# Kernel optimization log

Measured on AMD Instinct MI355X. Metric: run time of the kernel, lower is better.

Reference implementation:

```python
import jax, jax.numpy as jnp
import numpy as np

NUM_HEADS = 4
KEY_DIMS = 32  # c // num_heads


def rel_to_abs(x):
    # x: [B, N, W, 2W-1] relative logits -> [B, N, W, W] absolute logits
    b, n, w, _ = x.shape
    x = jnp.pad(x, ((0, 0), (0, 0), (0, 0), (0, 1)))           # [b,n,w,2w]
    x = x.reshape(b, n, w * 2 * w)
    x = jnp.pad(x, ((0, 0), (0, 0), (0, w - 1)))
    x = x.reshape(b, n, w + 1, 2 * w - 1)
    return x[:, :, :w, w - 1:]


def rel_logits_1d(q, rel_k):
    # q: [B, heads, X, Y, d], rel_k: [2Y-1, d] -> [B, heads, X, X, Y, Y]
    b, nh, xx, yy, d = q.shape
    rl = jnp.einsum('bhxyd,md->bhxym', q, rel_k)               # [b,h,x,y,2y-1]
    rl = rel_to_abs(rl.reshape(b, nh * xx, yy, 2 * yy - 1))    # [b,h*x,y,y]
    rl = rl.reshape(b, nh, xx, 1, yy, yy)
    return jnp.broadcast_to(rl, (b, nh, xx, xx, yy, yy))


def relative_position_bias(pos_q, pos_emb_h, pos_emb_w):
    # pos_q: [B, heads, H, W, d] -> bias [B, heads, H, W, H, W]
    rw = rel_logits_1d(pos_q, pos_emb_w)                        # [b,h,H,H,W,W]
    rw = rw.transpose(0, 1, 2, 4, 3, 5)                         # [b,h,H,W,H,W]
    rh = rel_logits_1d(pos_q.transpose(0, 1, 3, 2, 4), pos_emb_h)  # [b,h,W,W,H,H]
    rh = rh.transpose(0, 1, 4, 2, 5, 3)                         # [b,h,H,W,H,W]
    return rw + rh


def setup_inputs() -> dict:
    key = jax.random.key(0)
    k1, k2, k3, k4 = jax.random.split(key, 4)
    B, H, W, C = 2, 64, 64, 128
    qk_dims = NUM_HEADS * KEY_DIMS  # 128
    out_channels = C
    x = jax.random.normal(k1, (B, H, W, C), dtype=jnp.float32)
    w_qkv = jax.random.normal(k2, (C, 2 * qk_dims + out_channels), dtype=jnp.float32) * 0.05
    pos_emb_h = jax.random.normal(k3, (2 * H - 1, KEY_DIMS), dtype=jnp.float32) * 0.05
    pos_emb_w = jax.random.normal(k4, (2 * W - 1, KEY_DIMS), dtype=jnp.float32) * 0.05
    return {'x': x, 'w_qkv': w_qkv, 'pos_emb_h': pos_emb_h, 'pos_emb_w': pos_emb_w}


def reference(x, w_qkv, pos_emb_h, pos_emb_w):
    B, H, W, C = x.shape
    nh, kd = NUM_HEADS, KEY_DIMS
    qk_dims = nh * kd
    oc = C
    scale = 1.0 / float(kd) ** 0.5

    qkv = jnp.einsum('bhwc,cd->bhwd', x, w_qkv)                 # 1x1 conv, no bias
    q, k, v = jnp.split(qkv, [qk_dims, 2 * qk_dims], axis=-1)
    L = H * W
    q = q.reshape(B, L, nh, kd).transpose(0, 2, 1, 3)           # [B,nh,L,kd]
    k = k.reshape(B, L, nh, kd).transpose(0, 2, 1, 3)           # [B,nh,L,kd]
    v = v.reshape(B, L, nh, oc // nh).transpose(0, 2, 1, 3)     # [B,nh,L,dv]

    pos_q = q.reshape(B, nh, H, W, kd)
    pos = relative_position_bias(pos_q, pos_emb_h, pos_emb_w).reshape(B, nh, L, L)

    scores = jnp.einsum('bnqd,bnkd->bnqk', q, k) * scale + pos  # [B,nh,L,L]
    attn = jax.nn.softmax(scores, axis=-1)
    out = jnp.einsum('bnqk,bnkd->bnqd', attn, v)                # [B,nh,L,dv]
    out = out.transpose(0, 2, 1, 3).reshape(B, H, W, oc)
    return out
```

## Files before the change

### kernel.cpp

```cpp
#include <hip/hip_runtime.h>
#include <hip/hip_bf16.h>
#include <math.h>

#define B_  2
#define NH  4
#define HH  64
#define WW  64
#define KD  32
#define L_  4096
#define BN_ 8
#define LOG2E 1.4426950408889634f
#define KSCALE (0.17677669529663687f * 1.4426950408889634f)
#define FIXED_M 10.0f

typedef float    f32x4  __attribute__((ext_vector_type(4), may_alias));
typedef _Float16 half8  __attribute__((ext_vector_type(8), may_alias));
typedef _Float16 half4  __attribute__((ext_vector_type(4), may_alias));
typedef __fp16   fp16x2 __attribute__((ext_vector_type(2)));
typedef unsigned uint4v __attribute__((ext_vector_type(4), may_alias));

__device__ __forceinline__ float fexp2(float x) {
#if __has_builtin(__builtin_amdgcn_exp2f)
    return __builtin_amdgcn_exp2f(x);
#else
    return __expf(x * 0.69314718056f);
#endif
}

__device__ __forceinline__ unsigned pack2u(float a, float b) {
    fp16x2 t = __builtin_amdgcn_cvt_pkrtz(a, b);
    union { fp16x2 i; unsigned o; } u;
    u.i = t;
    return u.o;
}

__global__ __launch_bounds__(256) void qkv_gemm(const float* __restrict__ x,
                                                const float* __restrict__ w,
                                                _Float16* __restrict__ q_h,
                                                _Float16* __restrict__ k_h,
                                                _Float16* __restrict__ vt_h) {
    __shared__ __align__(16) char smem[34816];
    _Float16* xs  = (_Float16*)smem;
    _Float16* wsT = (_Float16*)(smem + 17408);

    const int mt = blockIdx.x % 128;
    const int nt = blockIdx.x / 128;
    const int m0 = mt * 64, n0 = nt * 64;
    const int tid = threadIdx.x;
    const int wv = tid >> 6, lane = tid & 63;
    const int l16 = lane & 15, quad = lane >> 4;

    #pragma unroll
    for (int i = 0; i < 8; i++) {
        const int idx = i * 256 + tid;
        const int row = idx >> 5, c4 = (idx & 31) * 4;
        const float4 v = *(const float4*)&x[(size_t)(m0 + row) * 128 + c4];
        half4 h;
        h[0] = (_Float16)v.x; h[1] = (_Float16)v.y;
        h[2] = (_Float16)v.z; h[3] = (_Float16)v.w;
        *(half4*)&xs[row * 136 + c4] = h;
    }
    #pragma unroll
    for (int i = 0; i < 8; i++) {
        const int idx = i * 256 + tid;
        const int k = idx >> 4, c4 = (idx & 15) * 4;
        const float4 v = *(const float4*)&w[(size_t)k * 384 + n0 + c4];
        wsT[(c4 + 0) * 136 + k] = (_Float16)v.x;
        wsT[(c4 + 1) * 136 + k] = (_Float16)v.y;
        wsT[(c4 + 2) * 136 + k] = (_Float16)v.z;
        wsT[(c4 + 3) * 136 + k] = (_Float16)v.w;
    }
    __syncthreads();

    f32x4 acc[4] = {{0.f,0.f,0.f,0.f},{0.f,0.f,0.f,0.f},
                    {0.f,0.f,0.f,0.f},{0.f,0.f,0.f,0.f}};
    half8 af[4];
    #pragma unroll
    for (int kc = 0; kc < 4; kc++)
        af[kc] = *(const half8*)&xs[(wv * 16 + l16) * 136 + kc * 32 + quad * 8];
    #pragma unroll
    for (int ns = 0; ns < 4; ns++)
        #pragma unroll
        for (int kc = 0; kc < 4; kc++) {
            const half8 bf = *(const half8*)&wsT[(ns * 16 + l16) * 136 + kc * 32 + quad * 8];
            acc[ns] = __builtin_amdgcn_mfma_f32_16x16x32_f16(af[kc], bf, acc[ns], 0, 0, 0);
        }

    const int which = n0 >> 7;
    const int nc = n0 & 127;
    const int b = m0 >> 12;
    if (which < 2) {
        _Float16* dst = (which == 0) ? q_h : k_h;
        const float mult = (which == 1) ? KSCALE : 1.0f;
        #pragma unroll
        for (int ns = 0; ns < 4; ns++) {
            const int col = nc + ns * 16 + l16;
            const int bn = b * NH + (col >> 5);
            const int d = col & 31;
            #pragma unroll
            for (int r = 0; r < 4; r++) {
                const int l = (m0 & 4095) + wv * 16 + quad * 4 + r;
                dst[((size_t)bn * L_ + l) * 32 + d] = (_Float16)(acc[ns][r] * mult);
            }
        }
    } else {
        __syncthreads();
        float* img = (float*)smem;
        #pragma unroll
        for (int ns = 0; ns < 4; ns++) {
            const int chan = ns * 16 + l16;
            const int h = chan >> 5, d = chan & 31;
            #pragma unroll
            for (int r = 0; r < 4; r++) {
                const int p = wv * 16 + quad * 4 + r;
                const int y = p >> 5, p32 = p & 31;
                const int q4 = (p32 >> 2) & 3;
                const int j = ((p32 >> 4) & 1) * 4 + (p32 & 3);
                const int fidx = h * 2048 + (y * 2 + (d >> 4)) * 512
                               + (q4 * 16 + (d & 15)) * 8 + j;
                img[fidx + (fidx >> 4)] = acc[ns][r];
            }
        }
        __syncthreads();
        const int ktg = (m0 & 4095) >> 6;
        #pragma unroll
        for (int h = 0; h < 2; h++) {
            const int head = (nc >> 5) + h;
            const int bn = b * NH + head;
            const int fbase = h * 2048 + tid * 8;
            const int sbase = fbase + (fbase >> 4);
            half8 o;
            #pragma unroll
            for (int e = 0; e < 8; e++) o[e] = (_Float16)img[sbase + e];
            *(half8*)(vt_h + (size_t)bn * 131072 + ktg * 2048 + tid * 8) = o;
        }
    }
}

__global__ __launch_bounds__(1024) void attn_mfma(
    const _Float16* __restrict__ q_h,
    const _Float16* __restrict__ k_h,
    const _Float16* __restrict__ vt_h,
    const float* __restrict__ emb_h,
    const float* __restrict__ emb_w,
    float* __restrict__ out)
{
    __shared__ __align__(16) char smem[66048];

    const int bi    = blockIdx.x;
    const int bn    = bi & 7;
    const int wpair = bi >> 3;
    const int tid   = threadIdx.x;
    const int wv    = tid >> 6;
    const int kh    = wv >> 3;
    const int ws    = wv & 7;
    const int qg    = ws >> 1;
    const int wo    = ws & 1;
    const int w1    = wpair * 2 + wo;
    const int lane  = tid & 63;
    const int l16   = lane & 15;
    const int quad  = lane >> 4;
    const int q0    = qg * 16;

    const _Float16* Kbase = k_h  + (size_t)bn * L_ * 32;
    const _Float16* Vtile = vt_h + (size_t)bn * 131072;

    const int Tt  = wv & 3;
    const int sC  = wv >> 2;
    const int khT = Tt & 1;
    const int isV = Tt >> 1;
    const _Float16* gstage = (isV ? Vtile : Kbase)
                           + (size_t)khT * 32 * 2048 + sC * 512 + lane * 8;
    const int ldsT = khT * 4096 + (isV
        ? (8192 + sC * 1024 + lane * 16)
        : ((sC * 16 + (lane >> 2)) * 64 + (((lane & 3) ^ ((lane >> 3) & 3)) << 4)));

    const uint4v stg0 = *(const uint4v*)gstage;

    float* Rw = (float*)(smem + 32768) + ws * 1040;

    const half8 aq = *(const half8*)(q_h +
        (((size_t)bn * L_ + (q0 + l16) * 64 + w1) * 32 + quad * 8));

    f32x4 qwT[4];
    #pragma unroll
    for (int sub = 0; sub < 4; sub++) {
        const float* ew = emb_w + (size_t)(sub * 16 + l16 - w1 + 63) * 32 + quad * 8;
        const float4 e0 = *(const float4*)ew;
        const float4 e1 = *(const float4*)(ew + 4);
        union { uint4v u; half8 h; } ua;
        ua.u[0] = pack2u(e0.x * LOG2E, e0.y * LOG2E);
        ua.u[1] = pack2u(e0.z * LOG2E, e0.w * LOG2E);
        ua.u[2] = pack2u(e1.x * LOG2E, e1.y * LOG2E);
        ua.u[3] = pack2u(e1.z * LOG2E, e1.w * LOG2E);
        f32x4 z = {-FIXED_M, -FIXED_M, -FIXED_M, -FIXED_M};
        qwT[sub] = __builtin_amdgcn_mfma_f32_16x16x32_f16(ua.h, aq, z, 0, 0, 0);
    }

    #pragma unroll
    for (int ji = 0; ji < 4; ji++) {
        const int jt = kh * 4 + ji;
        const int j = min(jt * 16 + l16, 126);
        const float* eh = emb_h + (size_t)j * 32 + quad * 8;
        const float4 e0 = *(const float4*)eh;
        const float4 e1 = *(const float4*)(eh + 4);
        union { uint4v u; half8 h; } ub;
        ub.u[0] = pack2u(e0.x * LOG2E, e0.y * LOG2E);
        ub.u[1] = pack2u(e0.z * LOG2E, e0.w * LOG2E);
        ub.u[2] = pack2u(e1.x * LOG2E, e1.y * LOG2E);
        ub.u[3] = pack2u(e1.z * LOG2E, e1.w * LOG2E);
        f32x4 z = {0.f, 0.f, 0.f, 0.f};
        const f32x4 C = __builtin_amdgcn_mfma_f32_16x16x32_f16(aq, ub.h, z, 0, 0, 0);
        #pragma unroll
        for (int r = 0; r < 4; r++) {
            const int row = quad * 4 + r;
            const int c = jt * 16 + l16 - 63 + (q0 + row);
            if (c >= 0 && c < 64)
                Rw[row * 65 + c] = C[r];
        }
    }

    *(uint4v*)(smem + ldsT) = stg0;
    __syncthreads();

    f32x4 O0 = {0.f, 0.f, 0.f, 0.f}, O1 = {0.f, 0.f, 0.f, 0.f};
    float l0 = 0.f, l1 = 0.f;
    const float* qh_row = Rw + l16 * 65;
    float qh_cur = qh_row[kh * 32];
#if __has_builtin(__builtin_amdgcn_fdot2)
    fp16x2 onep;
    { union { unsigned u; fp16x2 h; } uo; uo.u = pack2u(1.0f, 1.0f); onep = uo.h; }
#endif

    const int kOff = kh * 4096 + l16 * 64 + ((quad ^ ((l16 >> 1) & 3)) << 4);
    const int vOff = 8192 + kh * 4096 + lane * 16;

    #pragma unroll 2
    for (int t = 0; t < 32; t++) {
        const int cur = t & 1;
        const int tS = (t < 31) ? (t + 1) : 31;
        const uint4v stg = *(const uint4v*)(gstage + (size_t)tS * 2048);

        const char* kb = smem + cur * 16384 + kOff;
        const char* vb = smem + cur * 16384 + vOff;
        const half8 kf0 = *(const half8*)(kb);
        const half8 kf1 = *(const half8*)(kb + 1024);
        const half8 kf2 = *(const half8*)(kb + 2048);
        const half8 kf3 = *(const half8*)(kb + 3072);
        const half8 va00 = *(const half8*)(vb);
        const half8 va10 = *(const half8*)(vb + 1024);
        const half8 va01 = *(const half8*)(vb + 2048);
        const half8 va11 = *(const half8*)(vb + 3072);

        const f32x4 S0 = __builtin_amdgcn_mfma_f32_16x16x32_f16(kf0, aq, qwT[0], 0, 0, 0);
        const f32x4 S1 = __builtin_amdgcn_mfma_f32_16x16x32_f16(kf1, aq, qwT[1], 0, 0, 0);
        const f32x4 S2 = __builtin_amdgcn_mfma_f32_16x16x32_f16(kf2, aq, qwT[2], 0, 0, 0);
        const f32x4 S3 = __builtin_amdgcn_mfma_f32_16x16x32_f16(kf3, aq, qwT[3], 0, 0, 0);

        const float qh_next = qh_row[kh * 32 + tS];

        union { uint4v u; half8 h; } pb0, pb1;
        const float a0 = fexp2(S0[0] + qh_cur), a1 = fexp2(S0[1] + qh_cur);
        const float a2 = fexp2(S0[2] + qh_cur), a3 = fexp2(S0[3] + qh_cur);
        const float a4 = fexp2(S1[0] + qh_cur), a5 = fexp2(S1[1] + qh_cur);
        const float a6 = fexp2(S1[2] + qh_cur), a7 = fexp2(S1[3] + qh_cur);
        pb0.u[0] = pack2u(a0, a1); pb0.u[1] = pack2u(a2, a3);
        pb0.u[2] = pack2u(a4, a5); pb0.u[3] = pack2u(a6, a7);
        const float b0 = fexp2(S2[0] + qh_cur), b1 = fexp2(S2[1] + qh_cur);
        const float b2 = fexp2(S2[2] + qh_cur), b3 = fexp2(S2[3] + qh_cur);
        const float b4 = fexp2(S3[0] + qh_cur), b5 = fexp2(S3[1] + qh_cur);
        const float b6 = fexp2(S3[2] + qh_cur), b7 = fexp2(S3[3] + qh_cur);
        pb1.u[0] = pack2u(b0, b1); pb1.u[1] = pack2u(b2, b3);
        pb1.u[2] = pack2u(b4, b5); pb1.u[3] = pack2u(b6, b7);

        O0 = __builtin_amdgcn_mfma_f32_16x16x32_f16(va00, pb0.h, O0, 0, 0, 0);
        O0 = __builtin_amdgcn_mfma_f32_16x16x32_f16(va01, pb1.h, O0, 0, 0, 0);
        O1 = __builtin_amdgcn_mfma_f32_16x16x32_f16(va10, pb0.h, O1, 0, 0, 0);
        O1 = __builtin_amdgcn_mfma_f32_16x16x32_f16(va11, pb1.h, O1, 0, 0, 0);

#if __has_builtin(__builtin_amdgcn_fdot2)
        {
            union { unsigned u; fp16x2 h; } c0, c1, c2, c3;
            c0.u = pb0.u[0]; c1.u = pb0.u[1]; c2.u = pb0.u[2]; c3.u = pb0.u[3];
            l0 = __builtin_amdgcn_fdot2(c0.h, onep, l0, false);
            l0 = __builtin_amdgcn_fdot2(c1.h, onep, l0, false);
            l0 = __builtin_amdgcn_fdot2(c2.h, onep, l0, false);
            l0 = __builtin_amdgcn_fdot2(c3.h, onep, l0, false);
            c0.u = pb1.u[0]; c1.u = pb1.u[1]; c2.u = pb1.u[2]; c3.u = pb1.u[3];
            l1 = __builtin_amdgcn_fdot2(c0.h, onep, l1, false);
            l1 = __builtin_amdgcn_fdot2(c1.h, onep, l1, false);
            l1 = __builtin_amdgcn_fdot2(c2.h, onep, l1, false);
            l1 = __builtin_amdgcn_fdot2(c3.h, onep, l1, false);
        }
#else
        l0 += ((a0 + a1) + (a2 + a3)) + ((a4 + a5) + (a6 + a7));
        l1 += ((b0 + b1) + (b2 + b3)) + ((b4 + b5) + (b6 + b7));
#endif
        qh_cur = qh_next;

        __builtin_amdgcn_sched_barrier(0);
        *(uint4v*)(smem + (cur ^ 1) * 16384 + ldsT) = stg;
        __syncthreads();
    }

    float l = l0 + l1;
    l += __shfl_xor(l, 16);
    l += __shfl_xor(l, 32);

    __syncthreads();
    float (*mO)[32][17] = (float(*)[32][17])smem;
    float* mL = (float*)(smem + 34816);
    #pragma unroll
    for (int r = 0; r < 4; r++) {
        mO[wv][quad * 4 + r][l16]      = O0[r];
        mO[wv][16 + quad * 4 + r][l16] = O1[r];
    }
    if (quad == 0) mL[wv * 16 + l16] = l;
    __syncthreads();

    const int wo_o = tid >> 9;
    const int rest = tid & 511;
    const int h1   = rest >> 3;
    const int dg   = rest & 7;
    const int qgo  = h1 >> 4, ql = h1 & 15;
    const int wsA  = qgo * 2 + wo_o;
    const int wsB  = wsA + 8;
    const float denom = mL[wsA * 16 + ql] + mL[wsB * 16 + ql];
    const float inv = 1.0f / denom;
    float4 o;
    o.x = (mO[wsA][dg * 4 + 0][ql] + mO[wsB][dg * 4 + 0][ql]) * inv;
    o.y = (mO[wsA][dg * 4 + 1][ql] + mO[wsB][dg * 4 + 1][ql]) * inv;
    o.z = (mO[wsA][dg * 4 + 2][ql] + mO[wsB][dg * 4 + 2][ql]) * inv;
    o.w = (mO[wsA][dg * 4 + 3][ql] + mO[wsB][dg * 4 + 3][ql]) * inv;
    const int head = bn & 3, bb = bn >> 2;
    const int w1o = wpair * 2 + wo_o;
    *(float4*)&out[(((size_t)bb * 64 + h1) * 64 + w1o) * 128 + head * 32 + dg * 4] = o;
}

extern "C" void kernel_launch(void* const* d_in, const int* in_sizes, int n_in,
                              void* d_out, int out_size, void* d_ws, size_t ws_size,
                              hipStream_t stream) {
    const float* x     = (const float*)d_in[0];
    const float* w_qkv = (const float*)d_in[1];
    const float* emb_h = (const float*)d_in[2];
    const float* emb_w = (const float*)d_in[3];
    float* out = (float*)d_out;

    _Float16* q_h  = (_Float16*)d_ws;
    _Float16* k_h  = q_h + (size_t)BN_ * L_ * KD;
    _Float16* vt_h = k_h + (size_t)BN_ * L_ * KD;

    qkv_gemm<<<768, 256, 0, stream>>>(x, w_qkv, q_h, k_h, vt_h);
    attn_mfma<<<256, 1024, 0, stream>>>(q_h, k_h, vt_h, emb_h, emb_w, out);
}
```

Before: 107.2 us.

## Split attention blocks to one query column each with 512 threads

Each attention block now handles a single query column (w1) with 8 waves instead of two columns with 16 waves. The launch doubles to 512 blocks of 512 threads, and each thread stages two K/V chunks per iteration instead of one. Shared memory drops because only four Rw buffers are needed. The aim is more blocks to spread across CUs and better occupancy. In exchange, every K/V tile is loaded from global memory twice as often, since it is now shared by one column rather than two.

```diff
diff --git a/kernel.cpp b/kernel.cpp
--- a/kernel.cpp
+++ b/kernel.cpp
@@ -137,7 +137,7 @@
     }
 }
 
-__global__ __launch_bounds__(1024) void attn_mfma(
+__global__ __launch_bounds__(512) void attn_mfma(
     const _Float16* __restrict__ q_h,
     const _Float16* __restrict__ k_h,
     const _Float16* __restrict__ vt_h,
@@ -145,18 +145,15 @@
     const float* __restrict__ emb_w,
     float* __restrict__ out)
 {
-    __shared__ __align__(16) char smem[66048];
+    __shared__ __align__(16) char smem[49408];
 
     const int bi    = blockIdx.x;
     const int bn    = bi & 7;
-    const int wpair = bi >> 3;
+    const int w1    = bi >> 3;
     const int tid   = threadIdx.x;
     const int wv    = tid >> 6;
-    const int kh    = wv >> 3;
-    const int ws    = wv & 7;
-    const int qg    = ws >> 1;
-    const int wo    = ws & 1;
-    const int w1    = wpair * 2 + wo;
+    const int qg    = wv & 3;
+    const int kh    = wv >> 2;
     const int lane  = tid & 63;
     const int l16   = lane & 15;
     const int quad  = lane >> 4;
@@ -166,18 +163,25 @@
     const _Float16* Vtile = vt_h + (size_t)bn * 131072;
 
     const int Tt  = wv & 3;
-    const int sC  = wv >> 2;
+    const int sH  = wv >> 2;
     const int khT = Tt & 1;
     const int isV = Tt >> 1;
-    const _Float16* gstage = (isV ? Vtile : Kbase)
-                           + (size_t)khT * 32 * 2048 + sC * 512 + lane * 8;
-    const int ldsT = khT * 4096 + (isV
-        ? (8192 + sC * 1024 + lane * 16)
-        : ((sC * 16 + (lane >> 2)) * 64 + (((lane & 3) ^ ((lane >> 3) & 3)) << 4)));
-
-    const uint4v stg0 = *(const uint4v*)gstage;
-
-    float* Rw = (float*)(smem + 32768) + ws * 1040;
+    const _Float16* gs[2];
+    int ldsT[2];
+    #pragma unroll
+    for (int u = 0; u < 2; u++) {
+        const int sC = sH * 2 + u;
+        gs[u] = (isV ? Vtile : Kbase)
+              + (size_t)khT * 32 * 2048 + sC * 512 + lane * 8;
+        ldsT[u] = khT * 4096 + (isV
+            ? (8192 + sC * 1024 + lane * 16)
+            : ((sC * 16 + (lane >> 2)) * 64 + (((lane & 3) ^ ((lane >> 3) & 3)) << 4)));
+    }
+
+    const uint4v stg0a = *(const uint4v*)gs[0];
+    const uint4v stg0b = *(const uint4v*)gs[1];
+
+    float* Rw = (float*)(smem + 32768) + qg * 1040;
 
     const half8 aq = *(const half8*)(q_h +
         (((size_t)bn * L_ + (q0 + l16) * 64 + w1) * 32 + quad * 8));
@@ -220,7 +224,8 @@
         }
     }
 
-    *(uint4v*)(smem + ldsT) = stg0;
+    *(uint4v*)(smem + ldsT[0]) = stg0a;
+    *(uint4v*)(smem + ldsT[1]) = stg0b;
     __syncthreads();
 
     f32x4 O0 = {0.f, 0.f, 0.f, 0.f}, O1 = {0.f, 0.f, 0.f, 0.f};
@@ -239,7 +244,8 @@
     for (int t = 0; t < 32; t++) {
         const int cur = t & 1;
         const int tS = (t < 31) ? (t + 1) : 31;
-        const uint4v stg = *(const uint4v*)(gstage + (size_t)tS * 2048);
+        const uint4v sa = *(const uint4v*)(gs[0] + (size_t)tS * 2048);
+        const uint4v sb = *(const uint4v*)(gs[1] + (size_t)tS * 2048);
 
         const char* kb = smem + cur * 16384 + kOff;
         const char* vb = smem + cur * 16384 + vOff;
@@ -299,7 +305,8 @@
         qh_cur = qh_next;
 
         __builtin_amdgcn_sched_barrier(0);
-        *(uint4v*)(smem + (cur ^ 1) * 16384 + ldsT) = stg;
+        *(uint4v*)(smem + (cur ^ 1) * 16384 + ldsT[0]) = sa;
+        *(uint4v*)(smem + (cur ^ 1) * 16384 + ldsT[1]) = sb;
         __syncthreads();
     }
 
@@ -309,7 +316,7 @@
 
     __syncthreads();
     float (*mO)[32][17] = (float(*)[32][17])smem;
-    float* mL = (float*)(smem + 34816);
+    float* mL = (float*)(smem + 17408);
     #pragma unroll
     for (int r = 0; r < 4; r++) {
         mO[wv][quad * 4 + r][l16]      = O0[r];
@@ -318,13 +325,11 @@
     if (quad == 0) mL[wv * 16 + l16] = l;
     __syncthreads();
 
-    const int wo_o = tid >> 9;
-    const int rest = tid & 511;
-    const int h1   = rest >> 3;
-    const int dg   = rest & 7;
-    const int qgo  = h1 >> 4, ql = h1 & 15;
-    const int wsA  = qgo * 2 + wo_o;
-    const int wsB  = wsA + 8;
+    const int h1 = tid >> 3;
+    const int dg = tid & 7;
+    const int qgo = h1 >> 4, ql = h1 & 15;
+    const int wsA = qgo;
+    const int wsB = qgo + 4;
     const float denom = mL[wsA * 16 + ql] + mL[wsB * 16 + ql];
     const float inv = 1.0f / denom;
     float4 o;
@@ -333,8 +338,7 @@
     o.z = (mO[wsA][dg * 4 + 2][ql] + mO[wsB][dg * 4 + 2][ql]) * inv;
     o.w = (mO[wsA][dg * 4 + 3][ql] + mO[wsB][dg * 4 + 3][ql]) * inv;
     const int head = bn & 3, bb = bn >> 2;
-    const int w1o = wpair * 2 + wo_o;
-    *(float4*)&out[(((size_t)bb * 64 + h1) * 64 + w1o) * 128 + head * 32 + dg * 4] = o;
+    *(float4*)&out[(((size_t)bb * 64 + h1) * 64 + w1) * 128 + head * 32 + dg * 4] = o;
 }
 
 extern "C" void kernel_launch(void* const* d_in, const int* in_sizes, int n_in,
@@ -351,5 +355,5 @@
     _Float16* vt_h = k_h + (size_t)BN_ * L_ * KD;
 
     qkv_gemm<<<768, 256, 0, stream>>>(x, w_qkv, q_h, k_h, vt_h);
-    attn_mfma<<<256, 1024, 0, stream>>>(q_h, k_h, vt_h, emb_h, emb_w, out);
-}
+    attn_mfma<<<512, 512, 0, stream>>>(q_h, k_h, vt_h, emb_h, emb_w, out);
+}
```

Measured after the change: 104.4 us. 2.6% less time.

## Stage two key tiles per barrier and interleave softmax with MFMA across them

Applied to the files above, without the earlier changes.

Each loop iteration now stages and processes two 16-key tiles per head half instead of one. This halves the trip count and the number of block-wide __syncthreads. The exp2 softmax work for the first tile is interleaved with the score MFMAs of the second tile to overlap VALU and matrix work. Shared memory grows to hold the larger double buffer, and register pressure rises from the extra fragments.

```diff
diff --git a/kernel.cpp b/kernel.cpp
--- a/kernel.cpp
+++ b/kernel.cpp
@@ -145,7 +145,7 @@
     const float* __restrict__ emb_w,
     float* __restrict__ out)
 {
-    __shared__ __align__(16) char smem[66048];
+    __shared__ __align__(16) char smem[98816];
 
     const int bi    = blockIdx.x;
     const int bn    = bi & 7;
@@ -169,15 +169,24 @@
     const int sC  = wv >> 2;
     const int khT = Tt & 1;
     const int isV = Tt >> 1;
-    const _Float16* gstage = (isV ? Vtile : Kbase)
-                           + (size_t)khT * 32 * 2048 + sC * 512 + lane * 8;
-    const int ldsT = khT * 4096 + (isV
-        ? (8192 + sC * 1024 + lane * 16)
-        : ((sC * 16 + (lane >> 2)) * 64 + (((lane & 3) ^ ((lane >> 3) & 3)) << 4)));
-
-    const uint4v stg0 = *(const uint4v*)gstage;
-
-    float* Rw = (float*)(smem + 32768) + ws * 1040;
+    const _Float16* gs[2];
+    int ldsT[2];
+    #pragma unroll
+    for (int u = 0; u < 2; u++) {
+        const int cc = 2 * sC + u;
+        gs[u] = (isV ? Vtile : Kbase)
+              + (size_t)khT * 65536 + cc * 512 + lane * 8;
+        const int tile = cc >> 2;
+        const int c4   = cc & 3;
+        ldsT[u] = khT * 8192 + isV * 16384 + tile * 4096 + (isV
+            ? (c4 * 1024 + lane * 16)
+            : ((c4 * 16 + (lane >> 2)) * 64 + (((lane & 3) ^ ((lane >> 3) & 3)) << 4)));
+    }
+
+    const uint4v stg0a = *(const uint4v*)gs[0];
+    const uint4v stg0b = *(const uint4v*)gs[1];
+
+    float* Rw = (float*)(smem + 65536) + ws * 1040;
 
     const half8 aq = *(const half8*)(q_h +
         (((size_t)bn * L_ + (q0 + l16) * 64 + w1) * 32 + quad * 8));
@@ -220,86 +229,137 @@
         }
     }
 
-    *(uint4v*)(smem + ldsT) = stg0;
+    *(uint4v*)(smem + ldsT[0]) = stg0a;
+    *(uint4v*)(smem + ldsT[1]) = stg0b;
     __syncthreads();
 
     f32x4 O0 = {0.f, 0.f, 0.f, 0.f}, O1 = {0.f, 0.f, 0.f, 0.f};
     float l0 = 0.f, l1 = 0.f;
     const float* qh_row = Rw + l16 * 65;
-    float qh_cur = qh_row[kh * 32];
 #if __has_builtin(__builtin_amdgcn_fdot2)
     fp16x2 onep;
     { union { unsigned u; fp16x2 h; } uo; uo.u = pack2u(1.0f, 1.0f); onep = uo.h; }
 #endif
 
-    const int kOff = kh * 4096 + l16 * 64 + ((quad ^ ((l16 >> 1) & 3)) << 4);
-    const int vOff = 8192 + kh * 4096 + lane * 16;
+    const int swz16 = ((quad ^ ((l16 >> 1) & 3)) << 4);
+    const int kOff = kh * 8192 + l16 * 64 + swz16;
+    const int vOff = 16384 + kh * 8192 + lane * 16;
 
     #pragma unroll 2
-    for (int t = 0; t < 32; t++) {
+    for (int t = 0; t < 16; t++) {
         const int cur = t & 1;
-        const int tS = (t < 31) ? (t + 1) : 31;
-        const uint4v stg = *(const uint4v*)(gstage + (size_t)tS * 2048);
-
-        const char* kb = smem + cur * 16384 + kOff;
-        const char* vb = smem + cur * 16384 + vOff;
-        const half8 kf0 = *(const half8*)(kb);
-        const half8 kf1 = *(const half8*)(kb + 1024);
-        const half8 kf2 = *(const half8*)(kb + 2048);
-        const half8 kf3 = *(const half8*)(kb + 3072);
-        const half8 va00 = *(const half8*)(vb);
-        const half8 va10 = *(const half8*)(vb + 1024);
-        const half8 va01 = *(const half8*)(vb + 2048);
-        const half8 va11 = *(const half8*)(vb + 3072);
-
-        const f32x4 S0 = __builtin_amdgcn_mfma_f32_16x16x32_f16(kf0, aq, qwT[0], 0, 0, 0);
-        const f32x4 S1 = __builtin_amdgcn_mfma_f32_16x16x32_f16(kf1, aq, qwT[1], 0, 0, 0);
-        const f32x4 S2 = __builtin_amdgcn_mfma_f32_16x16x32_f16(kf2, aq, qwT[2], 0, 0, 0);
-        const f32x4 S3 = __builtin_amdgcn_mfma_f32_16x16x32_f16(kf3, aq, qwT[3], 0, 0, 0);
-
-        const float qh_next = qh_row[kh * 32 + tS];
-
-        union { uint4v u; half8 h; } pb0, pb1;
-        const float a0 = fexp2(S0[0] + qh_cur), a1 = fexp2(S0[1] + qh_cur);
-        const float a2 = fexp2(S0[2] + qh_cur), a3 = fexp2(S0[3] + qh_cur);
-        const float a4 = fexp2(S1[0] + qh_cur), a5 = fexp2(S1[1] + qh_cur);
-        const float a6 = fexp2(S1[2] + qh_cur), a7 = fexp2(S1[3] + qh_cur);
-        pb0.u[0] = pack2u(a0, a1); pb0.u[1] = pack2u(a2, a3);
-        pb0.u[2] = pack2u(a4, a5); pb0.u[3] = pack2u(a6, a7);
-        const float b0 = fexp2(S2[0] + qh_cur), b1 = fexp2(S2[1] + qh_cur);
-        const float b2 = fexp2(S2[2] + qh_cur), b3 = fexp2(S2[3] + qh_cur);
-        const float b4 = fexp2(S3[0] + qh_cur), b5 = fexp2(S3[1] + qh_cur);
-        const float b6 = fexp2(S3[2] + qh_cur), b7 = fexp2(S3[3] + qh_cur);
-        pb1.u[0] = pack2u(b0, b1); pb1.u[1] = pack2u(b2, b3);
-        pb1.u[2] = pack2u(b4, b5); pb1.u[3] = pack2u(b6, b7);
-
-        O0 = __builtin_amdgcn_mfma_f32_16x16x32_f16(va00, pb0.h, O0, 0, 0, 0);
-        O0 = __builtin_amdgcn_mfma_f32_16x16x32_f16(va01, pb1.h, O0, 0, 0, 0);
-        O1 = __builtin_amdgcn_mfma_f32_16x16x32_f16(va10, pb0.h, O1, 0, 0, 0);
-        O1 = __builtin_amdgcn_mfma_f32_16x16x32_f16(va11, pb1.h, O1, 0, 0, 0);
+        const int tS = (t < 15) ? (t + 1) : 15;
+        const uint4v sa = *(const uint4v*)(gs[0] + (size_t)tS * 4096);
+        const uint4v sb = *(const uint4v*)(gs[1] + (size_t)tS * 4096);
+
+        const char* base = smem + cur * 32768;
+        const char* kbA = base + kOff;
+        const char* vbA = base + vOff;
+
+        const float qhA = qh_row[kh * 32 + 2 * t];
+        const float qhB = qh_row[kh * 32 + 2 * t + 1];
+
+        const half8 kfA0 = *(const half8*)(kbA);
+        const half8 kfA1 = *(const half8*)(kbA + 1024);
+        const half8 kfA2 = *(const half8*)(kbA + 2048);
+        const half8 kfA3 = *(const half8*)(kbA + 3072);
+        const half8 vaA00 = *(const half8*)(vbA);
+        const half8 vaA10 = *(const half8*)(vbA + 1024);
+        const half8 vaA01 = *(const half8*)(vbA + 2048);
+        const half8 vaA11 = *(const half8*)(vbA + 3072);
+
+        const f32x4 SA0 = __builtin_amdgcn_mfma_f32_16x16x32_f16(kfA0, aq, qwT[0], 0, 0, 0);
+        const f32x4 SA1 = __builtin_amdgcn_mfma_f32_16x16x32_f16(kfA1, aq, qwT[1], 0, 0, 0);
+        const f32x4 SA2 = __builtin_amdgcn_mfma_f32_16x16x32_f16(kfA2, aq, qwT[2], 0, 0, 0);
+        const f32x4 SA3 = __builtin_amdgcn_mfma_f32_16x16x32_f16(kfA3, aq, qwT[3], 0, 0, 0);
+
+        const char* kbB = kbA + 4096;
+        const char* vbB = vbA + 4096;
+        const half8 kfB0 = *(const half8*)(kbB);
+        const half8 kfB1 = *(const half8*)(kbB + 1024);
+        const half8 kfB2 = *(const half8*)(kbB + 2048);
+        const half8 kfB3 = *(const half8*)(kbB + 3072);
+        const half8 vaB00 = *(const half8*)(vbB);
+        const half8 vaB10 = *(const half8*)(vbB + 1024);
+        const half8 vaB01 = *(const half8*)(vbB + 2048);
+        const half8 vaB11 = *(const half8*)(vbB + 3072);
+
+        union { uint4v u; half8 h; } pA0, pA1;
+        {
+            const float a0 = fexp2(SA0[0] + qhA), a1 = fexp2(SA0[1] + qhA);
+            const float a2 = fexp2(SA0[2] + qhA), a3 = fexp2(SA0[3] + qhA);
+            const float a4 = fexp2(SA1[0] + qhA), a5 = fexp2(SA1[1] + qhA);
+            const float a6 = fexp2(SA1[2] + qhA), a7 = fexp2(SA1[3] + qhA);
+            pA0.u[0] = pack2u(a0, a1); pA0.u[1] = pack2u(a2, a3);
+            pA0.u[2] = pack2u(a4, a5); pA0.u[3] = pack2u(a6, a7);
+            const float b0 = fexp2(SA2[0] + qhA), b1 = fexp2(SA2[1] + qhA);
+            const float b2 = fexp2(SA2[2] + qhA), b3 = fexp2(SA2[3] + qhA);
+            const float b4 = fexp2(SA3[0] + qhA), b5 = fexp2(SA3[1] + qhA);
+            const float b6 = fexp2(SA3[2] + qhA), b7 = fexp2(SA3[3] + qhA);
+            pA1.u[0] = pack2u(b0, b1); pA1.u[1] = pack2u(b2, b3);
+            pA1.u[2] = pack2u(b4, b5); pA1.u[3] = pack2u(b6, b7);
+        }
+
+        const f32x4 SB0 = __builtin_amdgcn_mfma_f32_16x16x32_f16(kfB0, aq, qwT[0], 0, 0, 0);
+        const f32x4 SB1 = __builtin_amdgcn_mfma_f32_16x16x32_f16(kfB1, aq, qwT[1], 0, 0, 0);
+        const f32x4 SB2 = __builtin_amdgcn_mfma_f32_16x16x32_f16(kfB2, aq, qwT[2], 0, 0, 0);
+        const f32x4 SB3 = __builtin_amdgcn_mfma_f32_16x16x32_f16(kfB3, aq, qwT[3], 0, 0, 0);
+
+        O0 = __builtin_amdgcn_mfma_f32_16x16x32_f16(vaA00, pA0.h, O0, 0, 0, 0);
+        O0 = __builtin_amdgcn_mfma_f32_16x16x32_f16(vaA01, pA1.h, O0, 0, 0, 0);
+        O1 = __builtin_amdgcn_mfma_f32_16x16x32_f16(vaA10, pA0.h, O1, 0, 0, 0);
+        O1 = __builtin_amdgcn_mfma_f32_16x16x32_f16(vaA11, pA1.h, O1, 0, 0, 0);
+
+        union { uint4v u; half8 h; } pB0, pB1;
+        {
+            const float a0 = fexp2(SB0[0] + qhB), a1 = fexp2(SB0[1] + qhB);
+            const float a2 = fexp2(SB0[2] + qhB), a3 = fexp2(SB0[3] + qhB);
+            const float a4 = fexp2(SB1[0] + qhB), a5 = fexp2(SB1[1] + qhB);
+            const float a6 = fexp2(SB1[2] + qhB), a7 = fexp2(SB1[3] + qhB);
+            pB0.u[0] = pack2u(a0, a1); pB0.u[1] = pack2u(a2, a3);
+            pB0.u[2] = pack2u(a4, a5); pB0.u[3] = pack2u(a6, a7);
+            const float b0 = fexp2(SB2[0] + qhB), b1 = fexp2(SB2[1] + qhB);
+            const float b2 = fexp2(SB2[2] + qhB), b3 = fexp2(SB2[3] + qhB);
+            const float b4 = fexp2(SB3[0] + qhB), b5 = fexp2(SB3[1] + qhB);
+            const float b6 = fexp2(SB3[2] + qhB), b7 = fexp2(SB3[3] + qhB);
+            pB1.u[0] = pack2u(b0, b1); pB1.u[1] = pack2u(b2, b3);
+            pB1.u[2] = pack2u(b4, b5); pB1.u[3] = pack2u(b6, b7);
+        }
+
+        O0 = __builtin_amdgcn_mfma_f32_16x16x32_f16(vaB00, pB0.h, O0, 0, 0, 0);
+        O0 = __builtin_amdgcn_mfma_f32_16x16x32_f16(vaB01, pB1.h, O0, 0, 0, 0);
+        O1 = __builtin_amdgcn_mfma_f32_16x16x32_f16(vaB10, pB0.h, O1, 0, 0, 0);
+        O1 = __builtin_amdgcn_mfma_f32_16x16x32_f16(vaB11, pB1.h, O1, 0, 0, 0);
 
 #if __has_builtin(__builtin_amdgcn_fdot2)
         {
             union { unsigned u; fp16x2 h; } c0, c1, c2, c3;
-            c0.u = pb0.u[0]; c1.u = pb0.u[1]; c2.u = pb0.u[2]; c3.u = pb0.u[3];
+            c0.u = pA0.u[0]; c1.u = pA0.u[1]; c2.u = pA0.u[2]; c3.u = pA0.u[3];
             l0 = __builtin_amdgcn_fdot2(c0.h, onep, l0, false);
             l0 = __builtin_amdgcn_fdot2(c1.h, onep, l0, false);
             l0 = __builtin_amdgcn_fdot2(c2.h, onep, l0, false);
             l0 = __builtin_amdgcn_fdot2(c3.h, onep, l0, false);
-            c0.u = pb1.u[0]; c1.u = pb1.u[1]; c2.u = pb1.u[2]; c3.u = pb1.u[3];
+            c0.u = pA1.u[0]; c1.u = pA1.u[1]; c2.u = pA1.u[2]; c3.u = pA1.u[3];
             l1 = __builtin_amdgcn_fdot2(c0.h, onep, l1, false);
             l1 = __builtin_amdgcn_fdot2(c1.h, onep, l1, false);
             l1 = __builtin_amdgcn_fdot2(c2.h, onep, l1, false);
             l1 = __builtin_amdgcn_fdot2(c3.h, onep, l1, false);
-        }
-#else
-        l0 += ((a0 + a1) + (a2 + a3)) + ((a4 + a5) + (a6 + a7));
-        l1 += ((b0 + b1) + (b2 + b3)) + ((b4 + b5) + (b6 + b7));
+            c0.u = pB0.u[0]; c1.u = pB0.u[1]; c2.u = pB0.u[2]; c3.u = pB0.u[3];
+            l0 = __builtin_amdgcn_fdot2(c0.h, onep, l0, false);
+            l0 = __builtin_amdgcn_fdot2(c1.h, onep, l0, false);
+            l0 = __builtin_amdgcn_fdot2(c2.h, onep, l0, false);
+            l0 = __builtin_amdgcn_fdot2(c3.h, onep, l0, false);
+            c0.u = pB1.u[0]; c1.u = pB1.u[1]; c2.u = pB1.u[2]; c3.u = pB1.u[3];
+            l1 = __builtin_amdgcn_fdot2(c0.h, onep, l1, false);
+            l1 = __builtin_amdgcn_fdot2(c1.h, onep, l1, false);
+            l1 = __builtin_amdgcn_fdot2(c2.h, onep, l1, false);
+            l1 = __builtin_amdgcn_fdot2(c3.h, onep, l1, false);
+        }
 #endif
-        qh_cur = qh_next;
 
         __builtin_amdgcn_sched_barrier(0);
-        *(uint4v*)(smem + (cur ^ 1) * 16384 + ldsT) = stg;
+        *(uint4v*)(smem + (cur ^ 1) * 32768 + ldsT[0]) = sa;
+        *(uint4v*)(smem + (cur ^ 1) * 32768 + ldsT[1]) = sb;
         __syncthreads();
     }
 
```

After: 101.2 us. -5.6%, faster.
